# Kernel tuning notes

Measured on AMD Instinct MI355X. Metric: run time of the kernel, lower is better.

Reference implementation:

```python
import jax, jax.numpy as jnp
import numpy as np

N_NODES = 100000
SELF_LOOP_W = 2.0  # improved=True in PyG GCNConv -> self-loop fill value 2.0


def gcn_conv(x, src, dst, ew, W, b, n_nodes):
    """PyG GCNConv (improved=True): x' = D^-1/2 (A + 2I) D^-1/2 (x W) + b."""
    h = x @ W  # [N, out]
    loop = jnp.arange(n_nodes, dtype=src.dtype)
    src_f = jnp.concatenate([src, loop])
    dst_f = jnp.concatenate([dst, loop])
    ew_f = jnp.concatenate([ew, jnp.full((n_nodes,), SELF_LOOP_W, dtype=ew.dtype)])
    deg = jax.ops.segment_sum(ew_f, dst_f, num_segments=n_nodes)  # [N]
    dinv = jnp.where(deg > 0, jax.lax.rsqrt(jnp.where(deg > 0, deg, 1.0)), 0.0)
    norm = dinv[src_f] * ew_f * dinv[dst_f]  # [E+N]
    msg = h[src_f] * norm[:, None]  # [E+N, out]
    out = jax.ops.segment_sum(msg, dst_f, num_segments=n_nodes)
    return out + b


def setup_inputs() -> dict:
    key = jax.random.key(0)
    k1, k2, k3, k4, k5 = jax.random.split(key, 5)
    N, E = N_NODES, 3200000
    F0, F1, F2 = 128, 128, 64
    x = jax.random.normal(k1, (N, F0), dtype=jnp.float32)
    edges = jax.random.randint(k2, (2, E), 0, N, dtype=jnp.int64)
    weights = jax.random.uniform(k3, (E,), dtype=jnp.float32)
    # kaiming_uniform on weight of shape [out, in]; stored transposed for x @ W
    bnd0 = float(np.sqrt(6.0 / F0))
    bnd1 = float(np.sqrt(6.0 / F1))
    W0 = jax.random.uniform(k4, (F0, F1), dtype=jnp.float32, minval=-bnd0, maxval=bnd0)
    W1 = jax.random.uniform(k5, (F1, F2), dtype=jnp.float32, minval=-bnd1, maxval=bnd1)
    b0 = jnp.zeros((F1,), dtype=jnp.float32)
    b1 = jnp.zeros((F2,), dtype=jnp.float32)
    return {"x": x, "edges": edges, "weights": weights,
            "W0": W0, "b0": b0, "W1": W1, "b1": b1}


def reference(x, edges, weights, W0, b0, W1, b1):
    src, dst = edges[0], edges[1]
    n = x.shape[0]
    h = gcn_conv(x, src, dst, weights, W0, b0, n)
    h = jax.nn.relu(h)
    h = gcn_conv(h, src, dst, weights, W1, b1, n)
    return jax.nn.sigmoid(h)
```

## Files before the change

### kernel.cpp

```cpp
#include <hip/hip_runtime.h>
#include <math.h>

typedef __attribute__((ext_vector_type(8))) short bf16x8;
typedef __attribute__((ext_vector_type(4))) float f32x4;

#define NBLK 1024
#define GB   16
#define BPG  (NBLK / GB)


__device__ __forceinline__ unsigned short f2b(float f) {
  unsigned u = __float_as_uint(f);
  unsigned r = u + 0x7fffu + ((u >> 16) & 1u);
  return (unsigned short)(r >> 16);
}
__device__ __forceinline__ float b2f_lo(unsigned v) {
  return __uint_as_float(v << 16);
}
__device__ __forceinline__ float b2f_hi(unsigned v) {
  return __uint_as_float(v & 0xffff0000u);
}


__global__ __launch_bounds__(256) void bucket_hist(const int* __restrict__ dst,
                                                   int* __restrict__ blkhist,
                                                   int NB, int E, int chunk) {
  extern __shared__ int sm_hist[];
  for (int i = threadIdx.x; i < NB; i += 256) sm_hist[i] = 0;
  __syncthreads();
  const int b = blockIdx.x;
  const int beg = b * chunk;
  const int end = min(E, beg + chunk);
  int j = beg + threadIdx.x * 4;
  for (; j + 4 <= end; j += 1024) {
    const int4 d4 = *(const int4*)&dst[j];
    atomicAdd(&sm_hist[d4.x >> 8], 1);
    atomicAdd(&sm_hist[d4.y >> 8], 1);
    atomicAdd(&sm_hist[d4.z >> 8], 1);
    atomicAdd(&sm_hist[d4.w >> 8], 1);
  }
  for (; j < end; j += 1024) {
    const int lim = min(j + 4, end);
    for (int t2 = j; t2 < lim; ++t2) atomicAdd(&sm_hist[dst[t2] >> 8], 1);
  }
  __syncthreads();
  for (int i = threadIdx.x; i < NB; i += 256) blkhist[(long)b * NB + i] = sm_hist[i];
}

__global__ __launch_bounds__(256) void col_part(const int* __restrict__ blkhist,
                                                int* __restrict__ partials, int NB) {
  const int k = blockIdx.x * 256 + threadIdx.x;
  const int g = blockIdx.y;
  if (k >= NB) return;
  const long base = (long)g * BPG * NB + k;
  int sum = 0;
  int i = 0;
  for (; i + 4 <= BPG; i += 4) {
    const int t0 = blkhist[base + (long)(i + 0) * NB];
    const int t1 = blkhist[base + (long)(i + 1) * NB];
    const int t2 = blkhist[base + (long)(i + 2) * NB];
    const int t3 = blkhist[base + (long)(i + 3) * NB];
    sum += t0 + t1 + t2 + t3;
  }
  for (; i < BPG; ++i) sum += blkhist[base + (long)i * NB];
  partials[(long)g * NB + k] = sum;
}

__global__ __launch_bounds__(256) void col_scan16(int* __restrict__ partials,
                                                  int* __restrict__ bstart, int NB) {
  const int k = blockIdx.x * 256 + threadIdx.x;
  if (k >= NB) return;
  int run = 0;
#pragma unroll
  for (int g = 0; g < GB; ++g) {
    const int t = partials[(long)g * NB + k];
    partials[(long)g * NB + k] = run;
    run += t;
  }
  bstart[k] = run;
}

__global__ __launch_bounds__(256) void col_apply(int* __restrict__ blkhist,
                                                 const int* __restrict__ partials,
                                                 int NB) {
  const int k = blockIdx.x * 256 + threadIdx.x;
  const int g = blockIdx.y;
  if (k >= NB) return;
  const long base = (long)g * BPG * NB + k;
  int run = partials[(long)g * NB + k];
  int i = 0;
  for (; i + 4 <= BPG; i += 4) {
    const int t0 = blkhist[base + (long)(i + 0) * NB];
    const int t1 = blkhist[base + (long)(i + 1) * NB];
    const int t2 = blkhist[base + (long)(i + 2) * NB];
    const int t3 = blkhist[base + (long)(i + 3) * NB];
    blkhist[base + (long)(i + 0) * NB] = run; run += t0;
    blkhist[base + (long)(i + 1) * NB] = run; run += t1;
    blkhist[base + (long)(i + 2) * NB] = run; run += t2;
    blkhist[base + (long)(i + 3) * NB] = run; run += t3;
  }
  for (; i < BPG; ++i) {
    const int t = blkhist[base + (long)i * NB];
    blkhist[base + (long)i * NB] = run;
    run += t;
  }
}

__global__ __launch_bounds__(256) void scan_single(int* __restrict__ cr, int n) {
  __shared__ int sm[256];
  __shared__ int sbase;
  if (threadIdx.x == 0) sbase = 0;
  __syncthreads();
  for (int c0 = 0; c0 < n; c0 += 256) {
    const int i = c0 + threadIdx.x;
    const int v = (i < n) ? cr[i] : 0;
    sm[threadIdx.x] = v;
    __syncthreads();
    for (int off = 1; off < 256; off <<= 1) {
      int a = (threadIdx.x >= off) ? sm[threadIdx.x - off] : 0;
      __syncthreads();
      sm[threadIdx.x] += a;
      __syncthreads();
    }
    const int b = sbase;
    const int tot = sm[255];
    if (i < n) cr[i] = b + sm[threadIdx.x] - v;
    __syncthreads();
    if (threadIdx.x == 0) sbase = b + tot;
    __syncthreads();
  }
  if (threadIdx.x == 0) cr[n] = sbase;
}

__global__ __launch_bounds__(256) void bucket_scatter(const int* __restrict__ src,
                                                      const int* __restrict__ dst,
                                                      const float* __restrict__ ew,
                                                      const int* __restrict__ blkhist,
                                                      const int* __restrict__ bstart,
                                                      uint2* __restrict__ bkt, int NB,
                                                      int E, int chunk) {
  extern __shared__ int sm_cur[];
  const int b = blockIdx.x;
  for (int i = threadIdx.x; i < NB; i += 256)
    sm_cur[i] = blkhist[(long)b * NB + i] + bstart[i];
  __syncthreads();
  const int beg = b * chunk;
  const int end = min(E, beg + chunk);
  int j = beg + threadIdx.x * 4;
  for (; j + 4 <= end; j += 1024) {
    const int4 d4 = *(const int4*)&dst[j];
    const int4 s4 = *(const int4*)&src[j];
    const float4 e4 = *(const float4*)&ew[j];
    int q0 = (int)(e4.x * 32767.f + 0.5f); q0 = (q0 < 0) ? 0 : ((q0 > 32767) ? 32767 : q0);
    int q1 = (int)(e4.y * 32767.f + 0.5f); q1 = (q1 < 0) ? 0 : ((q1 > 32767) ? 32767 : q1);
    int q2 = (int)(e4.z * 32767.f + 0.5f); q2 = (q2 < 0) ? 0 : ((q2 > 32767) ? 32767 : q2);
    int q3 = (int)(e4.w * 32767.f + 0.5f); q3 = (q3 < 0) ? 0 : ((q3 > 32767) ? 32767 : q3);
    const int p0 = atomicAdd(&sm_cur[d4.x >> 8], 1);
    bkt[p0] = make_uint2(((unsigned)s4.x << 15) | (unsigned)q0, (unsigned)(d4.x & 255));
    const int p1 = atomicAdd(&sm_cur[d4.y >> 8], 1);
    bkt[p1] = make_uint2(((unsigned)s4.y << 15) | (unsigned)q1, (unsigned)(d4.y & 255));
    const int p2 = atomicAdd(&sm_cur[d4.z >> 8], 1);
    bkt[p2] = make_uint2(((unsigned)s4.z << 15) | (unsigned)q2, (unsigned)(d4.z & 255));
    const int p3 = atomicAdd(&sm_cur[d4.w >> 8], 1);
    bkt[p3] = make_uint2(((unsigned)s4.w << 15) | (unsigned)q3, (unsigned)(d4.w & 255));
  }
  for (; j < end; j += 1024) {
    const int lim = min(j + 4, end);
    for (int t2 = j; t2 < lim; ++t2) {
      const int d = dst[t2];
      int q = (int)(ew[t2] * 32767.f + 0.5f);
      q = (q < 0) ? 0 : ((q > 32767) ? 32767 : q);
      const unsigned rec = ((unsigned)src[t2] << 15) | (unsigned)q;
      const int pos = atomicAdd(&sm_cur[d >> 8], 1);
      bkt[pos] = make_uint2(rec, (unsigned)(d & 255));
    }
  }
}

__global__ __launch_bounds__(256) void bucket_finalize(const uint2* __restrict__ bkt,
                                                       const int* __restrict__ bstart,
                                                       unsigned* __restrict__ recs,
                                                       int* __restrict__ row_start,
                                                       float* __restrict__ dinv, int NB,
                                                       int N, int E) {
  __shared__ int hist[256], qs[256], cur[256], lstart[256];
  const int k = blockIdx.x;
  const int t = threadIdx.x;
  hist[t] = 0;
  qs[t] = 0;
  __syncthreads();
  const int beg = bstart[k], end = bstart[k + 1];
  for (int j = beg + t; j < end; j += 256) {
    const uint2 v = bkt[j];
    atomicAdd(&hist[v.y], 1);
    atomicAdd(&qs[v.y], (int)(v.x & 32767u));
  }
  __syncthreads();
  if (t == 0) {
    int run = 0;
    for (int i = 0; i < 256; ++i) { lstart[i] = run; run += hist[i]; }
  }
  __syncthreads();
  cur[t] = lstart[t];
  const int node = k * 256 + t;
  if (node < N) {
    row_start[node] = beg + lstart[t];
    dinv[node] = rsqrtf((float)qs[t] * (1.f / 32767.f) + 2.0f);
  }
  if (k == NB - 1 && t == 0) row_start[N] = E;
  __syncthreads();
  for (int j = beg + t; j < end; j += 256) {
    const uint2 v = bkt[j];
    const int off = atomicAdd(&cur[v.y], 1);
    recs[beg + off] = v.x;
  }
}


__global__ __launch_bounds__(256) void fold_dinv(unsigned int* __restrict__ recs,
                                                 const float* __restrict__ dinv, int E) {
  const int i4 = (blockIdx.x * 256 + threadIdx.x) * 4;
  if (i4 + 4 <= E) {
    uint4 r = *(uint4*)&recs[i4];
    const float v0 = (float)(r.x & 32767u) * (1.f / 32767.f) * dinv[r.x >> 15];
    const float v1 = (float)(r.y & 32767u) * (1.f / 32767.f) * dinv[r.y >> 15];
    const float v2 = (float)(r.z & 32767u) * (1.f / 32767.f) * dinv[r.z >> 15];
    const float v3 = (float)(r.w & 32767u) * (1.f / 32767.f) * dinv[r.w >> 15];
    int q0 = (int)(v0 * (32767.f / 0.75f) + 0.5f); q0 = (q0 > 32767) ? 32767 : q0;
    int q1 = (int)(v1 * (32767.f / 0.75f) + 0.5f); q1 = (q1 > 32767) ? 32767 : q1;
    int q2 = (int)(v2 * (32767.f / 0.75f) + 0.5f); q2 = (q2 > 32767) ? 32767 : q2;
    int q3 = (int)(v3 * (32767.f / 0.75f) + 0.5f); q3 = (q3 > 32767) ? 32767 : q3;
    r.x = (r.x & ~32767u) | (unsigned)q0;
    r.y = (r.y & ~32767u) | (unsigned)q1;
    r.z = (r.z & ~32767u) | (unsigned)q2;
    r.w = (r.w & ~32767u) | (unsigned)q3;
    *(uint4*)&recs[i4] = r;
  } else {
    for (int i = i4; i < E; ++i) {
      const unsigned rec = recs[i];
      const int s = rec >> 15;
      const float v = (float)(rec & 32767u) * (1.f / 32767.f) * dinv[s];
      int q = (int)(v * (32767.f / 0.75f) + 0.5f);
      q = (q > 32767) ? 32767 : q;
      recs[i] = ((unsigned)s << 15) | (unsigned)q;
    }
  }
}


__global__ __launch_bounds__(256) void to_bf16_8(const float* __restrict__ x,
                                                 unsigned short* __restrict__ xb,
                                                 int n8) {
  int i = blockIdx.x * 256 + threadIdx.x;
  if (i >= n8) return;
  const float4 a = *(const float4*)&x[(long)i * 8];
  const float4 b = *(const float4*)&x[(long)i * 8 + 4];
  uint4 o;
  o.x = (unsigned)f2b(a.x) | ((unsigned)f2b(a.y) << 16);
  o.y = (unsigned)f2b(a.z) | ((unsigned)f2b(a.w) << 16);
  o.z = (unsigned)f2b(b.x) | ((unsigned)f2b(b.y) << 16);
  o.w = (unsigned)f2b(b.z) | ((unsigned)f2b(b.w) << 16);
  *(uint4*)&xb[(long)i * 8] = o;
}

__global__ __launch_bounds__(256) void pack_wfrag(const float* __restrict__ W,
                                                  unsigned short* __restrict__ frag,
                                                  int C, int total) {
  int i = blockIdx.x * 256 + threadIdx.x;
  if (i >= total) return;
  const int e = i & 7;
  const int lane = (i >> 3) & 63;
  const int t = i >> 9;
  const int kk = t & 3;
  const int ct = t >> 2;
  const int k = kk * 32 + (lane >> 4) * 8 + e;
  const int c = ct * 16 + (lane & 15);
  frag[i] = f2b(W[(long)k * C + c]);
}


__global__ __launch_bounds__(256) void gather_l1_half(const uint4* __restrict__ xb4,
                                                      const unsigned int* __restrict__ recs,
                                                      const int* __restrict__ row_start,
                                                      const float* __restrict__ dinv,
                                                      uint4* __restrict__ xab4, int N,
                                                      int half) {
  const int t = blockIdx.x * 256 + threadIdx.x;
  const int d = t >> 3;
  if (d >= N) return;
  const int jl = (t & 7) + half * 8;
  const int beg = row_start[d], end = row_start[d + 1];
  const float dd = dinv[d];
  constexpr float S = 0.75f / 32767.f;
  const uint4 sv = xb4[(long)d * 16 + jl];
  const float sl = 2.f * dd * dd;
  float aca[8], acb[8];
  aca[0] = b2f_lo(sv.x) * sl; aca[1] = b2f_hi(sv.x) * sl;
  aca[2] = b2f_lo(sv.y) * sl; aca[3] = b2f_hi(sv.y) * sl;
  aca[4] = b2f_lo(sv.z) * sl; aca[5] = b2f_hi(sv.z) * sl;
  aca[6] = b2f_lo(sv.w) * sl; aca[7] = b2f_hi(sv.w) * sl;
#pragma unroll
  for (int u = 0; u < 8; ++u) acb[u] = 0.f;
  int j = beg;
  for (; j + 8 <= end; j += 8) {
    unsigned rr[8];
    uint4 vv[8];
#pragma unroll
    for (int u = 0; u < 8; ++u) rr[u] = recs[j + u];
#pragma unroll
    for (int u = 0; u < 8; ++u) vv[u] = xb4[(long)(rr[u] >> 15) * 16 + jl];
#pragma unroll
    for (int u = 0; u < 8; ++u) {
      const float cf = (float)(rr[u] & 32767u) * S * dd;
      float* ac = (u & 1) ? acb : aca;
      ac[0] = fmaf(cf, b2f_lo(vv[u].x), ac[0]);
      ac[1] = fmaf(cf, b2f_hi(vv[u].x), ac[1]);
      ac[2] = fmaf(cf, b2f_lo(vv[u].y), ac[2]);
      ac[3] = fmaf(cf, b2f_hi(vv[u].y), ac[3]);
      ac[4] = fmaf(cf, b2f_lo(vv[u].z), ac[4]);
      ac[5] = fmaf(cf, b2f_hi(vv[u].z), ac[5]);
      ac[6] = fmaf(cf, b2f_lo(vv[u].w), ac[6]);
      ac[7] = fmaf(cf, b2f_hi(vv[u].w), ac[7]);
    }
  }
  for (; j < end; ++j) {
    const unsigned rec = recs[j];
    const uint4 v = xb4[(long)(rec >> 15) * 16 + jl];
    const float cf = (float)(rec & 32767u) * S * dd;
    aca[0] = fmaf(cf, b2f_lo(v.x), aca[0]);
    aca[1] = fmaf(cf, b2f_hi(v.x), aca[1]);
    aca[2] = fmaf(cf, b2f_lo(v.y), aca[2]);
    aca[3] = fmaf(cf, b2f_hi(v.y), aca[3]);
    aca[4] = fmaf(cf, b2f_lo(v.z), aca[4]);
    aca[5] = fmaf(cf, b2f_hi(v.z), aca[5]);
    aca[6] = fmaf(cf, b2f_lo(v.w), aca[6]);
    aca[7] = fmaf(cf, b2f_hi(v.w), aca[7]);
  }
#pragma unroll
  for (int u = 0; u < 8; ++u) aca[u] += acb[u];
  uint4 o;
  o.x = (unsigned)f2b(aca[0]) | ((unsigned)f2b(aca[1]) << 16);
  o.y = (unsigned)f2b(aca[2]) | ((unsigned)f2b(aca[3]) << 16);
  o.z = (unsigned)f2b(aca[4]) | ((unsigned)f2b(aca[5]) << 16);
  o.w = (unsigned)f2b(aca[6]) | ((unsigned)f2b(aca[7]) << 16);
  xab4[(long)d * 16 + jl] = o;
}


__global__ __launch_bounds__(256) void fused_mlp_mfma(
    const unsigned short* __restrict__ xab, const unsigned short* __restrict__ w0f,
    const float* __restrict__ b0, const unsigned short* __restrict__ w1f,
    unsigned short* __restrict__ r2b, int N) {
  __shared__ unsigned short Hl[4][16][136];
  const int tid = threadIdx.x;
  const int w = tid >> 6, l = tid & 63;
  const int lr = l & 15, lg = l >> 4;
  const int row0 = blockIdx.x * 64 + w * 16;

  int arow = row0 + lr;
  if (arow >= N) arow = N - 1;
  const unsigned short* ap = xab + (long)arow * 128 + lg * 8;
  const bf16x8 a0 = *(const bf16x8*)(ap);
  const bf16x8 a1 = *(const bf16x8*)(ap + 32);
  const bf16x8 a2 = *(const bf16x8*)(ap + 64);
  const bf16x8 a3 = *(const bf16x8*)(ap + 96);

  for (int ct = 0; ct < 8; ++ct) {
    const unsigned short* bp = w0f + ct * 2048 + l * 8;
    f32x4 acc = {0.f, 0.f, 0.f, 0.f};
    acc = __builtin_amdgcn_mfma_f32_16x16x32_bf16(a0, *(const bf16x8*)(bp), acc, 0, 0, 0);
    acc = __builtin_amdgcn_mfma_f32_16x16x32_bf16(a1, *(const bf16x8*)(bp + 512), acc, 0, 0, 0);
    acc = __builtin_amdgcn_mfma_f32_16x16x32_bf16(a2, *(const bf16x8*)(bp + 1024), acc, 0, 0, 0);
    acc = __builtin_amdgcn_mfma_f32_16x16x32_bf16(a3, *(const bf16x8*)(bp + 1536), acc, 0, 0, 0);
    const float bv = b0[ct * 16 + lr];
#pragma unroll
    for (int r = 0; r < 4; ++r) {
      Hl[w][lg * 4 + r][ct * 16 + lr] = f2b(fmaxf(acc[r] + bv, 0.f));
    }
  }

  const unsigned short* hp = &Hl[w][lr][lg * 8];
  const bf16x8 h0 = *(const bf16x8*)(hp);
  const bf16x8 h1 = *(const bf16x8*)(hp + 32);
  const bf16x8 h2 = *(const bf16x8*)(hp + 64);
  const bf16x8 h3 = *(const bf16x8*)(hp + 96);

  for (int ct = 0; ct < 4; ++ct) {
    const unsigned short* bp = w1f + ct * 2048 + l * 8;
    f32x4 acc = {0.f, 0.f, 0.f, 0.f};
    acc = __builtin_amdgcn_mfma_f32_16x16x32_bf16(h0, *(const bf16x8*)(bp), acc, 0, 0, 0);
    acc = __builtin_amdgcn_mfma_f32_16x16x32_bf16(h1, *(const bf16x8*)(bp + 512), acc, 0, 0, 0);
    acc = __builtin_amdgcn_mfma_f32_16x16x32_bf16(h2, *(const bf16x8*)(bp + 1024), acc, 0, 0, 0);
    acc = __builtin_amdgcn_mfma_f32_16x16x32_bf16(h3, *(const bf16x8*)(bp + 1536), acc, 0, 0, 0);
#pragma unroll
    for (int r = 0; r < 4; ++r) {
      const int orow = row0 + lg * 4 + r;
      if (orow < N) r2b[(long)orow * 64 + ct * 16 + lr] = f2b(acc[r]);
    }
  }
}


__global__ __launch_bounds__(256) void gather_l2(const uint4* __restrict__ r2b4,
                                                 const unsigned int* __restrict__ recs,
                                                 const int* __restrict__ row_start,
                                                 const float* __restrict__ dinv,
                                                 const float* __restrict__ b1,
                                                 float* __restrict__ out, int N) {
  const int t = blockIdx.x * 256 + threadIdx.x;
  const int d = t >> 3;
  if (d >= N) return;
  const int jl = t & 7;
  const int beg = row_start[d], end = row_start[d + 1];
  const float dd = dinv[d];
  constexpr float S = 0.75f / 32767.f;
  const uint4 sv = r2b4[(long)d * 8 + jl];
  const float sl = 2.f * dd * dd;
  float aca[8], acb[8];
  aca[0] = b2f_lo(sv.x) * sl; aca[1] = b2f_hi(sv.x) * sl;
  aca[2] = b2f_lo(sv.y) * sl; aca[3] = b2f_hi(sv.y) * sl;
  aca[4] = b2f_lo(sv.z) * sl; aca[5] = b2f_hi(sv.z) * sl;
  aca[6] = b2f_lo(sv.w) * sl; aca[7] = b2f_hi(sv.w) * sl;
#pragma unroll
  for (int u = 0; u < 8; ++u) acb[u] = 0.f;
  int j = beg;
  for (; j + 8 <= end; j += 8) {
    unsigned rr[8];
    uint4 vv[8];
#pragma unroll
    for (int u = 0; u < 8; ++u) rr[u] = recs[j + u];
#pragma unroll
    for (int u = 0; u < 8; ++u) vv[u] = r2b4[(long)(rr[u] >> 15) * 8 + jl];
#pragma unroll
    for (int u = 0; u < 8; ++u) {
      const float cf = (float)(rr[u] & 32767u) * S * dd;
      float* ac = (u & 1) ? acb : aca;
      ac[0] = fmaf(cf, b2f_lo(vv[u].x), ac[0]);
      ac[1] = fmaf(cf, b2f_hi(vv[u].x), ac[1]);
      ac[2] = fmaf(cf, b2f_lo(vv[u].y), ac[2]);
      ac[3] = fmaf(cf, b2f_hi(vv[u].y), ac[3]);
      ac[4] = fmaf(cf, b2f_lo(vv[u].z), ac[4]);
      ac[5] = fmaf(cf, b2f_hi(vv[u].z), ac[5]);
      ac[6] = fmaf(cf, b2f_lo(vv[u].w), ac[6]);
      ac[7] = fmaf(cf, b2f_hi(vv[u].w), ac[7]);
    }
  }
  for (; j < end; ++j) {
    const unsigned rec = recs[j];
    const uint4 v = r2b4[(long)(rec >> 15) * 8 + jl];
    const float cf = (float)(rec & 32767u) * S * dd;
    aca[0] = fmaf(cf, b2f_lo(v.x), aca[0]);
    aca[1] = fmaf(cf, b2f_hi(v.x), aca[1]);
    aca[2] = fmaf(cf, b2f_lo(v.y), aca[2]);
    aca[3] = fmaf(cf, b2f_hi(v.y), aca[3]);
    aca[4] = fmaf(cf, b2f_lo(v.z), aca[4]);
    aca[5] = fmaf(cf, b2f_hi(v.z), aca[5]);
    aca[6] = fmaf(cf, b2f_lo(v.w), aca[6]);
    aca[7] = fmaf(cf, b2f_hi(v.w), aca[7]);
  }
#pragma unroll
  for (int u = 0; u < 8; ++u) aca[u] += acb[u];
  const int c = jl * 8;
  const float4 ba = *(const float4*)&b1[c];
  const float4 bb = *(const float4*)&b1[c + 4];
  float4 o1, o2;
  o1.x = 1.f / (1.f + __expf(-(aca[0] + ba.x)));
  o1.y = 1.f / (1.f + __expf(-(aca[1] + ba.y)));
  o1.z = 1.f / (1.f + __expf(-(aca[2] + ba.z)));
  o1.w = 1.f / (1.f + __expf(-(aca[3] + ba.w)));
  o2.x = 1.f / (1.f + __expf(-(aca[4] + bb.x)));
  o2.y = 1.f / (1.f + __expf(-(aca[5] + bb.y)));
  o2.z = 1.f / (1.f + __expf(-(aca[6] + bb.z)));
  o2.w = 1.f / (1.f + __expf(-(aca[7] + bb.w)));
  *(float4*)&out[(long)d * 64 + c] = o1;
  *(float4*)&out[(long)d * 64 + c + 4] = o2;
}


extern "C" void kernel_launch(void* const* d_in, const int* in_sizes, int n_in,
                              void* d_out, int out_size, void* d_ws, size_t ws_size,
                              hipStream_t stream) {
  const float* x  = (const float*)d_in[0];
  const int* src  = (const int*)d_in[1];
  const float* ew = (const float*)d_in[2];
  const float* W0 = (const float*)d_in[3];
  const float* b0 = (const float*)d_in[4];
  const float* W1 = (const float*)d_in[5];
  const float* b1 = (const float*)d_in[6];
  float* out = (float*)d_out;

  const int N = in_sizes[0] / 128;
  const int E = in_sizes[2];
  const int* dstp = src + E;

  const int NB = (N + 255) >> 8;
  const int chunk = (((E + NBLK - 1) / NBLK) + 3) & ~3;

  float* ws = (float*)d_ws;
  const size_t oN = ((size_t)N + 255) & ~(size_t)255;
  float* dinv = ws;
  int* rowst = (int*)(ws + oN);
  int* bstart = rowst + oN;
  int* partials = bstart + 2048;
  unsigned int* recs = (unsigned int*)(partials + 32768);
  unsigned int* xb = recs + E;
  uint2* bkt = (uint2*)xb;
  const size_t xb_units = ((size_t)2 * E > (size_t)N * 64) ? (size_t)2 * E : (size_t)N * 64;
  unsigned int* xab = xb + xb_units;
  int* blkhist = (int*)xab;
  unsigned short* w0f = (unsigned short*)(xab + (size_t)N * 64);
  unsigned short* w1f = w0f + 16384;
  unsigned int* r2b = xb;

  const int nblkB = (NB + 255) / 256;

  bucket_hist<<<NBLK, 256, NB * 4, stream>>>(dstp, blkhist, NB, E, chunk);
  col_part<<<dim3(nblkB, GB), 256, 0, stream>>>(blkhist, partials, NB);
  col_scan16<<<nblkB, 256, 0, stream>>>(partials, bstart, NB);
  col_apply<<<dim3(nblkB, GB), 256, 0, stream>>>(blkhist, partials, NB);
  scan_single<<<1, 256, 0, stream>>>(bstart, NB);
  bucket_scatter<<<NBLK, 256, NB * 4, stream>>>(src, dstp, ew, blkhist, bstart, bkt, NB,
                                                E, chunk);
  bucket_finalize<<<NB, 256, 0, stream>>>(bkt, bstart, recs, rowst, dinv, NB, N, E);
  fold_dinv<<<(E / 4 + 256) / 256, 256, 0, stream>>>(recs, dinv, E);

  pack_wfrag<<<64, 256, 0, stream>>>(W0, w0f, 128, 16384);
  pack_wfrag<<<32, 256, 0, stream>>>(W1, w1f, 64, 8192);
  to_bf16_8<<<(N * 16 + 255) / 256, 256, 0, stream>>>(x, (unsigned short*)xb, N * 16);

  const int gl1b = (N * 8 + 255) / 256;
  gather_l1_half<<<gl1b, 256, 0, stream>>>((const uint4*)xb, recs, rowst, dinv,
                                           (uint4*)xab, N, 0);
  gather_l1_half<<<gl1b, 256, 0, stream>>>((const uint4*)xb, recs, rowst, dinv,
                                           (uint4*)xab, N, 1);

  fused_mlp_mfma<<<(N + 63) / 64, 256, 0, stream>>>((const unsigned short*)xab, w0f, b0,
                                                    w1f, (unsigned short*)r2b, N);
  gather_l2<<<(N * 8 + 255) / 256, 256, 0, stream>>>((const uint4*)r2b, recs, rowst, dinv,
                                                     b1, out, N);
}
```

Before: 311.2 us.

## Locally sort edges by bucket in LDS before scattering to global buckets

The bucket scatter kernel now counts each block's per-bucket edge counts, scans them in LDS, and places edge indices into a block-local sorted array in shared memory. A second pass then reads edges in bucket order and writes packed records to consecutive global positions, so the global writes are coalesced instead of random. In exchange it adds a 512-element LDS scan, a second read of src/dst/ew through indirection, and about 16 KB of extra LDS per block (chunk is roughly 3128 ints), which may lower occupancy. It also assumes NB is at most 512 and that chunk fits in 16 bits.

```diff
diff --git a/kernel.cpp b/kernel.cpp
--- a/kernel.cpp
+++ b/kernel.cpp
@@ -67,7 +67,8 @@
 }
 
 __global__ __launch_bounds__(256) void col_scan16(int* __restrict__ partials,
-                                                  int* __restrict__ bstart, int NB) {
+                                                  int* __restrict__ bstart,
+                                                  int* __restrict__ coltot, int NB) {
   const int k = blockIdx.x * 256 + threadIdx.x;
   if (k >= NB) return;
   int run = 0;
@@ -78,6 +79,7 @@
     run += t;
   }
   bstart[k] = run;
+  coltot[k] = run;
 }
 
 __global__ __launch_bounds__(256) void col_apply(int* __restrict__ blkhist,
@@ -137,43 +139,78 @@
                                                       const float* __restrict__ ew,
                                                       const int* __restrict__ blkhist,
                                                       const int* __restrict__ bstart,
+                                                      const int* __restrict__ coltot,
                                                       uint2* __restrict__ bkt, int NB,
                                                       int E, int chunk) {
-  extern __shared__ int sm_cur[];
+  extern __shared__ int lds[];
+  int* A = lds;
+  int* L = lds + NB;
+  int* C = lds + NB + 512;
+  unsigned* SV = (unsigned*)(lds + 2 * NB + 512);
   const int b = blockIdx.x;
-  for (int i = threadIdx.x; i < NB; i += 256)
-    sm_cur[i] = blkhist[(long)b * NB + i] + bstart[i];
-  __syncthreads();
+  const int t = threadIdx.x;
   const int beg = b * chunk;
   const int end = min(E, beg + chunk);
-  int j = beg + threadIdx.x * 4;
+  const int total = end - beg;
+
+  for (int k = t; k < 512; k += 256) L[k] = 0;
+  __syncthreads();
+  for (int k = t; k < NB; k += 256) {
+    const int my = blkhist[(long)b * NB + k];
+    const int nxt = (b + 1 < (int)gridDim.x) ? blkhist[(long)(b + 1) * NB + k]
+                                             : coltot[k];
+    const int c = nxt - my;
+    A[k] = my + bstart[k];
+    C[k] = c;
+    L[k] = c;
+  }
+  __syncthreads();
+  for (int off = 1; off < 512; off <<= 1) {
+    const int a0 = (t >= off) ? L[t - off] : 0;
+    const int a1 = (256 + t >= off) ? L[256 + t - off] : 0;
+    __syncthreads();
+    L[t] += a0;
+    L[256 + t] += a1;
+    __syncthreads();
+  }
+  for (int k = t; k < NB; k += 256) {
+    const int ex = L[k] - C[k];
+    L[k] = ex;
+    C[k] = ex;
+  }
+  __syncthreads();
+  int j = beg + t * 4;
   for (; j + 4 <= end; j += 1024) {
     const int4 d4 = *(const int4*)&dst[j];
-    const int4 s4 = *(const int4*)&src[j];
-    const float4 e4 = *(const float4*)&ew[j];
-    int q0 = (int)(e4.x * 32767.f + 0.5f); q0 = (q0 < 0) ? 0 : ((q0 > 32767) ? 32767 : q0);
-    int q1 = (int)(e4.y * 32767.f + 0.5f); q1 = (q1 < 0) ? 0 : ((q1 > 32767) ? 32767 : q1);
-    int q2 = (int)(e4.z * 32767.f + 0.5f); q2 = (q2 < 0) ? 0 : ((q2 > 32767) ? 32767 : q2);
-    int q3 = (int)(e4.w * 32767.f + 0.5f); q3 = (q3 < 0) ? 0 : ((q3 > 32767) ? 32767 : q3);
-    const int p0 = atomicAdd(&sm_cur[d4.x >> 8], 1);
-    bkt[p0] = make_uint2(((unsigned)s4.x << 15) | (unsigned)q0, (unsigned)(d4.x & 255));
-    const int p1 = atomicAdd(&sm_cur[d4.y >> 8], 1);
-    bkt[p1] = make_uint2(((unsigned)s4.y << 15) | (unsigned)q1, (unsigned)(d4.y & 255));
-    const int p2 = atomicAdd(&sm_cur[d4.z >> 8], 1);
-    bkt[p2] = make_uint2(((unsigned)s4.z << 15) | (unsigned)q2, (unsigned)(d4.z & 255));
-    const int p3 = atomicAdd(&sm_cur[d4.w >> 8], 1);
-    bkt[p3] = make_uint2(((unsigned)s4.w << 15) | (unsigned)q3, (unsigned)(d4.w & 255));
+    const unsigned le = (unsigned)(j - beg);
+    const int p0 = atomicAdd(&C[d4.x >> 8], 1);
+    SV[p0] = ((unsigned)(d4.x >> 8) << 16) | le;
+    const int p1 = atomicAdd(&C[d4.y >> 8], 1);
+    SV[p1] = ((unsigned)(d4.y >> 8) << 16) | (le + 1);
+    const int p2 = atomicAdd(&C[d4.z >> 8], 1);
+    SV[p2] = ((unsigned)(d4.z >> 8) << 16) | (le + 2);
+    const int p3 = atomicAdd(&C[d4.w >> 8], 1);
+    SV[p3] = ((unsigned)(d4.w >> 8) << 16) | (le + 3);
   }
   for (; j < end; j += 1024) {
     const int lim = min(j + 4, end);
     for (int t2 = j; t2 < lim; ++t2) {
-      const int d = dst[t2];
-      int q = (int)(ew[t2] * 32767.f + 0.5f);
-      q = (q < 0) ? 0 : ((q > 32767) ? 32767 : q);
-      const unsigned rec = ((unsigned)src[t2] << 15) | (unsigned)q;
-      const int pos = atomicAdd(&sm_cur[d >> 8], 1);
-      bkt[pos] = make_uint2(rec, (unsigned)(d & 255));
-    }
+      const int p = atomicAdd(&C[dst[t2] >> 8], 1);
+      SV[p] = ((unsigned)(dst[t2] >> 8) << 16) | (unsigned)(t2 - beg);
+    }
+  }
+  __syncthreads();
+  for (int p = t; p < total; p += 256) {
+    const unsigned v = SV[p];
+    const int k = v >> 16;
+    const int le = v & 0xffffu;
+    const int d = dst[beg + le];
+    const int s = src[beg + le];
+    const float w = ew[beg + le];
+    int q = (int)(w * 32767.f + 0.5f);
+    q = (q < 0) ? 0 : ((q > 32767) ? 32767 : q);
+    bkt[A[k] + (p - L[k])] =
+        make_uint2(((unsigned)s << 15) | (unsigned)q, (unsigned)(d & 255));
   }
 }
 
@@ -501,6 +538,7 @@
   float* dinv = ws;
   int* rowst = (int*)(ws + oN);
   int* bstart = rowst + oN;
+  int* coltot = bstart + 1024;
   int* partials = bstart + 2048;
   unsigned int* recs = (unsigned int*)(partials + 32768);
   unsigned int* xb = recs + E;
@@ -516,11 +554,12 @@
 
   bucket_hist<<<NBLK, 256, NB * 4, stream>>>(dstp, blkhist, NB, E, chunk);
   col_part<<<dim3(nblkB, GB), 256, 0, stream>>>(blkhist, partials, NB);
-  col_scan16<<<nblkB, 256, 0, stream>>>(partials, bstart, NB);
+  col_scan16<<<nblkB, 256, 0, stream>>>(partials, bstart, coltot, NB);
   col_apply<<<dim3(nblkB, GB), 256, 0, stream>>>(blkhist, partials, NB);
   scan_single<<<1, 256, 0, stream>>>(bstart, NB);
-  bucket_scatter<<<NBLK, 256, NB * 4, stream>>>(src, dstp, ew, blkhist, bstart, bkt, NB,
-                                                E, chunk);
+  const int scat_lds = (2 * NB + 512 + chunk) * 4;
+  bucket_scatter<<<NBLK, 256, scat_lds, stream>>>(src, dstp, ew, blkhist, bstart, coltot,
+                                                  bkt, NB, E, chunk);
   bucket_finalize<<<NB, 256, 0, stream>>>(bkt, bstart, recs, rowst, dinv, NB, N, E);
   fold_dinv<<<(E / 4 + 256) / 256, 256, 0, stream>>>(recs, dinv, E);
 
```

New measurement: 321.8 us. +3.4%, slower.

## Sort nodes by degree within each bucket to balance gather wavefronts

Applied to the files above, without the earlier changes.

bucket_finalize now builds a per-256-node permutation that orders nodes by in-degree using a small shared-memory counting sort. The layer-1 and layer-2 gather kernels read their destination node through this permutation, so lanes in a wavefront handle nodes with similar edge counts and diverge less in their edge loops. This adds an extra indirection load per thread, scatters writes to output rows within each 256-node group, and adds a little work to finalize. With random edges the degree spread is modest (mean near 32), so the balancing benefit may be limited.

```diff
diff --git a/kernel.cpp b/kernel.cpp
--- a/kernel.cpp
+++ b/kernel.cpp
@@ -181,13 +181,15 @@
                                                        const int* __restrict__ bstart,
                                                        unsigned* __restrict__ recs,
                                                        int* __restrict__ row_start,
-                                                       float* __restrict__ dinv, int NB,
+                                                       float* __restrict__ dinv,
+                                                       int* __restrict__ perm, int NB,
                                                        int N, int E) {
-  __shared__ int hist[256], qs[256], cur[256], lstart[256];
+  __shared__ int hist[256], qs[256], cur[256], lstart[256], bh[256];
   const int k = blockIdx.x;
   const int t = threadIdx.x;
   hist[t] = 0;
   qs[t] = 0;
+  bh[t] = 0;
   __syncthreads();
   const int beg = bstart[k], end = bstart[k + 1];
   for (int j = beg + t; j < end; j += 256) {
@@ -196,11 +198,21 @@
     atomicAdd(&qs[v.y], (int)(v.x & 32767u));
   }
   __syncthreads();
+  const int deg = hist[t];
+  const int bin = (deg > 255) ? 255 : deg;
+  atomicAdd(&bh[bin], 1);
   if (t == 0) {
     int run = 0;
     for (int i = 0; i < 256; ++i) { lstart[i] = run; run += hist[i]; }
   }
   __syncthreads();
+  if (t == 0) {
+    int run = 0;
+    for (int i = 0; i < 256; ++i) { const int c = bh[i]; bh[i] = run; run += c; }
+  }
+  __syncthreads();
+  const int pos = atomicAdd(&bh[bin], 1);
+  perm[k * 256 + pos] = k * 256 + t;
   cur[t] = lstart[t];
   const int node = k * 256 + t;
   if (node < N) {
@@ -283,10 +295,13 @@
                                                       const unsigned int* __restrict__ recs,
                                                       const int* __restrict__ row_start,
                                                       const float* __restrict__ dinv,
+                                                      const int* __restrict__ perm,
                                                       uint4* __restrict__ xab4, int N,
-                                                      int half) {
+                                                      int NP, int half) {
   const int t = blockIdx.x * 256 + threadIdx.x;
-  const int d = t >> 3;
+  const int idx = t >> 3;
+  if (idx >= NP) return;
+  const int d = perm[idx];
   if (d >= N) return;
   const int jl = (t & 7) + half * 8;
   const int beg = row_start[d], end = row_start[d + 1];
@@ -405,10 +420,13 @@
                                                  const unsigned int* __restrict__ recs,
                                                  const int* __restrict__ row_start,
                                                  const float* __restrict__ dinv,
+                                                 const int* __restrict__ perm,
                                                  const float* __restrict__ b1,
-                                                 float* __restrict__ out, int N) {
+                                                 float* __restrict__ out, int N, int NP) {
   const int t = blockIdx.x * 256 + threadIdx.x;
-  const int d = t >> 3;
+  const int idx = t >> 3;
+  if (idx >= NP) return;
+  const int d = perm[idx];
   if (d >= N) return;
   const int jl = t & 7;
   const int beg = row_start[d], end = row_start[d + 1];
@@ -494,6 +512,7 @@
   const int* dstp = src + E;
 
   const int NB = (N + 255) >> 8;
+  const int NP = NB * 256;
   const int chunk = (((E + NBLK - 1) / NBLK) + 3) & ~3;
 
   float* ws = (float*)d_ws;
@@ -502,7 +521,8 @@
   int* rowst = (int*)(ws + oN);
   int* bstart = rowst + oN;
   int* partials = bstart + 2048;
-  unsigned int* recs = (unsigned int*)(partials + 32768);
+  int* perm = partials + 32768;
+  unsigned int* recs = (unsigned int*)(perm + NP);
   unsigned int* xb = recs + E;
   uint2* bkt = (uint2*)xb;
   const size_t xb_units = ((size_t)2 * E > (size_t)N * 64) ? (size_t)2 * E : (size_t)N * 64;
@@ -521,21 +541,21 @@
   scan_single<<<1, 256, 0, stream>>>(bstart, NB);
   bucket_scatter<<<NBLK, 256, NB * 4, stream>>>(src, dstp, ew, blkhist, bstart, bkt, NB,
                                                 E, chunk);
-  bucket_finalize<<<NB, 256, 0, stream>>>(bkt, bstart, recs, rowst, dinv, NB, N, E);
+  bucket_finalize<<<NB, 256, 0, stream>>>(bkt, bstart, recs, rowst, dinv, perm, NB, N, E);
   fold_dinv<<<(E / 4 + 256) / 256, 256, 0, stream>>>(recs, dinv, E);
 
   pack_wfrag<<<64, 256, 0, stream>>>(W0, w0f, 128, 16384);
   pack_wfrag<<<32, 256, 0, stream>>>(W1, w1f, 64, 8192);
   to_bf16_8<<<(N * 16 + 255) / 256, 256, 0, stream>>>(x, (unsigned short*)xb, N * 16);
 
-  const int gl1b = (N * 8 + 255) / 256;
-  gather_l1_half<<<gl1b, 256, 0, stream>>>((const uint4*)xb, recs, rowst, dinv,
-                                           (uint4*)xab, N, 0);
-  gather_l1_half<<<gl1b, 256, 0, stream>>>((const uint4*)xb, recs, rowst, dinv,
-                                           (uint4*)xab, N, 1);
+  const int gpb = NP / 32;
+  gather_l1_half<<<gpb, 256, 0, stream>>>((const uint4*)xb, recs, rowst, dinv, perm,
+                                          (uint4*)xab, N, NP, 0);
+  gather_l1_half<<<gpb, 256, 0, stream>>>((const uint4*)xb, recs, rowst, dinv, perm,
+                                          (uint4*)xab, N, NP, 1);
 
   fused_mlp_mfma<<<(N + 63) / 64, 256, 0, stream>>>((const unsigned short*)xab, w0f, b0,
                                                     w1f, (unsigned short*)r2b, N);
-  gather_l2<<<(N * 8 + 255) / 256, 256, 0, stream>>>((const uint4*)r2b, recs, rowst, dinv,
-                                                     b1, out, N);
-}
+  gather_l2<<<gpb, 256, 0, stream>>>((const uint4*)r2b, recs, rowst, dinv, perm, b1, out,
+                                     N, NP);
+}
```

After: 340.7 us. 1.09x slower.
